# Kernel tuning notes

Measured on AMD Instinct MI355X. Metric: run time of the kernel, lower is better.

## Reference

```python
import jax, jax.numpy as jnp
import numpy as np

D_MODEL = 1024
NUM_HEADS = 16
DEPTH = D_MODEL // NUM_HEADS
B, S = 2, 2048


def setup_inputs() -> dict:
    key = jax.random.key(0)
    ks = jax.random.split(key, 13)
    sc = 1.0 / np.sqrt(D_MODEL)
    inp = {
        "q": jax.random.normal(ks[0], (B, S, D_MODEL), jnp.float32),
        "k": jax.random.normal(ks[1], (B, S, D_MODEL), jnp.float32),
        "v": jax.random.normal(ks[2], (B, S, D_MODEL), jnp.float32),
        "mask": jax.random.randint(ks[3], (B, 1, S, S), 0, 2).astype(jnp.float32),
        "wq": jax.random.normal(ks[4], (D_MODEL, D_MODEL), jnp.float32) * sc,
        "bq": jnp.zeros((D_MODEL,), jnp.float32),
        "wk": jax.random.normal(ks[5], (D_MODEL, D_MODEL), jnp.float32) * sc,
        "bk": jnp.zeros((D_MODEL,), jnp.float32),
        "wv": jax.random.normal(ks[6], (D_MODEL, D_MODEL), jnp.float32) * sc,
        "bv": jnp.zeros((D_MODEL,), jnp.float32),
        "wo": jax.random.normal(ks[7], (D_MODEL, D_MODEL), jnp.float32) * sc,
        "bo": jnp.zeros((D_MODEL,), jnp.float32),
    }
    return inp


def _split_heads(x):
    # [B,S,D] -> [B,H,S,depth]
    b, s, _ = x.shape
    return x.reshape(b, s, NUM_HEADS, DEPTH).transpose(0, 2, 1, 3)


def reference(q, k, v, mask, wq, bq, wk, bk, wv, bv, wo, bo):
    qh = _split_heads(q @ wq.T + bq)
    kh = _split_heads(k @ wk.T + bk)
    vh = _split_heads(v @ wv.T + bv)
    logits = jnp.einsum("bhqd,bhkd->bhqk", qh, kh) / jnp.sqrt(
        jnp.asarray(DEPTH, jnp.float32))
    logits = logits + mask * (-1e9)
    attn = jax.nn.softmax(logits, axis=-1)
    out = jnp.einsum("bhqk,bhkd->bhqd", attn, vh)
    out = out.transpose(0, 2, 1, 3).reshape(q.shape[0], -1, D_MODEL)
    return out @ wo.T + bo
```

## Files before the change

### kernel.cpp

```cpp
#include <hip/hip_runtime.h>

#define D_MODEL 1024
#define NHEADS  16
#define DEPTH   64
#define BATCH   2
#define SEQ     2048
#define MROWS   (BATCH * SEQ)
#define QSCALE  0.18033688011112042f

typedef unsigned short u16;
typedef unsigned int   u32;
typedef unsigned long long u64;
typedef __bf16 bf16x8 __attribute__((ext_vector_type(8)));
typedef float  f32x4  __attribute__((ext_vector_type(4)));

#if __has_builtin(__builtin_amdgcn_exp2f)
#define EXP2(x) __builtin_amdgcn_exp2f(x)
#else
#define EXP2(x) exp2f(x)
#endif

__device__ __forceinline__ u16 f2b(float f) {
    return __builtin_bit_cast(u16, static_cast<__bf16>(f));
}
__device__ __forceinline__ bf16x8 ldb8(const u16* p) {
    return __builtin_bit_cast(bf16x8, *(const uint4*)p);
}
__device__ __forceinline__ void gload16(const u16* g, u16* l) {
    __builtin_amdgcn_global_load_lds(
        (const __attribute__((address_space(1))) void*)g,
        (__attribute__((address_space(3))) void*)l, 16, 0, 0);
}

__global__ __launch_bounds__(256) void pack_mask(
    const float* __restrict__ mask, u64* __restrict__ bits)
{
    const int w    = blockIdx.x * 4 + (threadIdx.x >> 6);
    const int lane = threadIdx.x & 63;
    float m = mask[(size_t)w * 64 + lane];
    u64 b = __ballot(m > 0.5f);
    if (lane == 0) bits[w] = b;
}

__global__ __launch_bounds__(256) void cvt_pack(
    const float* __restrict__ q, const float* __restrict__ k, const float* __restrict__ v,
    const float* __restrict__ wq, const float* __restrict__ wk, const float* __restrict__ wv,
    const float* __restrict__ wo, const float* __restrict__ mask,
    u16* __restrict__ xb, u16* __restrict__ wb, u64* __restrict__ bits)
{
    if (blockIdx.x >= 8192) {
        const int w    = (blockIdx.x - 8192) * 4 + (threadIdx.x >> 6);
        const int lane = threadIdx.x & 63;
        float m = mask[(size_t)w * 64 + lane];
        u64 b = __ballot(m > 0.5f);
        if (lane == 0) bits[w] = b;
        return;
    }
    const size_t e = ((size_t)blockIdx.x * 256 + threadIdx.x) * 8;
    const float* src;
    u16* dst;
    size_t off;
    if (e < 12582912) {
        const int a = (int)(e >> 22);
        off = e & 4194303;
        src = (a == 0) ? q : (a == 1) ? k : v;
        dst = xb + ((size_t)a << 22) + off;
    } else {
        const size_t e2 = e - 12582912;
        const int a = (int)(e2 >> 20);
        off = e2 & 1048575;
        src = (a == 0) ? wq : (a == 1) ? wk : (a == 2) ? wv : wo;
        dst = wb + ((size_t)a << 20) + off;
    }
    const float4 f0 = *(const float4*)(src + off);
    const float4 f1 = *(const float4*)(src + off + 4);
    uint4 o;
    o.x = (u32)f2b(f0.x) | ((u32)f2b(f0.y) << 16);
    o.y = (u32)f2b(f0.z) | ((u32)f2b(f0.w) << 16);
    o.z = (u32)f2b(f1.x) | ((u32)f2b(f1.y) << 16);
    o.w = (u32)f2b(f1.z) | ((u32)f2b(f1.w) << 16);
    *(uint4*)dst = o;
}

__global__ __launch_bounds__(256, 3) void proj3_bf16(
    const u16* __restrict__ xb, const u16* __restrict__ wb,
    const float* __restrict__ bq, const float* __restrict__ bk, const float* __restrict__ bv,
    u16* __restrict__ qws, u16* __restrict__ kws, u16* __restrict__ vtws)
{
    __shared__ __align__(16) u16 smem[16384];
    u16 (*la)[4096] = reinterpret_cast<u16(*)[4096]>(smem);
    u16 (*lb)[4096] = reinterpret_cast<u16(*)[4096]>(smem + 8192);

    const int z = blockIdx.z;
    const u16* X = xb + ((size_t)z << 22);
    const u16* W = wb + ((size_t)z << 20);
    const float* Bi = (z == 0) ? bq : (z == 1) ? bk : bv;
    u16* dst       = (z == 0) ? qws : (z == 1) ? kws : vtws;

    const int tid  = threadIdx.x;
    const int wv_  = tid >> 6;
    const int lane = tid & 63;
    const int quad = lane >> 4;
    const int l15  = lane & 15;
    const int bx = blockIdx.y >> 2;
    const int by = (blockIdx.x << 2) | (blockIdx.y & 3);
    const int wm = (wv_ >> 1) * 64;
    const int wn = (wv_ & 1) * 64;

    f32x4 acc[4][4];
    for (int i = 0; i < 4; ++i)
        for (int j = 0; j < 4; ++j)
            acc[i][j] = (f32x4){0.f, 0.f, 0.f, 0.f};

    const int rowA0 = by * 128;
    const int rowB0 = bx * 128;

    const int strow = tid >> 2;
    const int stcol = (tid & 3) * 8;
    const u16* gA0 = &X[(size_t)(rowA0 + strow) * D_MODEL + stcol];
    const u16* gA1 = gA0 + (size_t)64 * D_MODEL;
    const u16* gB0 = &W[(size_t)(rowB0 + strow) * D_MODEL + stcol];
    const u16* gB1 = gB0 + (size_t)64 * D_MODEL;
    const int l0 = tid * 8, l1 = 2048 + tid * 8;

    gload16(gA0, &la[0][l0]);
    gload16(gA1, &la[0][l1]);
    gload16(gB0, &lb[0][l0]);
    gload16(gB1, &lb[0][l1]);
    __syncthreads();

    for (int t = 0; t < 32; ++t) {
        const int buf = t & 1;
        if (t < 31) {
            const int ko = (t + 1) * 32;
            gload16(gA0 + ko, &la[buf ^ 1][l0]);
            gload16(gA1 + ko, &la[buf ^ 1][l1]);
            gload16(gB0 + ko, &lb[buf ^ 1][l0]);
            gload16(gB1 + ko, &lb[buf ^ 1][l1]);
        }
        bf16x8 af[4], bfr[4];
        #pragma unroll
        for (int tt = 0; tt < 4; ++tt) {
            af[tt]  = ldb8(&la[buf][(wm + tt * 16 + l15) * 32 + quad * 8]);
            bfr[tt] = ldb8(&lb[buf][(wn + tt * 16 + l15) * 32 + quad * 8]);
        }
        #pragma unroll
        for (int mt = 0; mt < 4; ++mt)
            #pragma unroll
            for (int nt = 0; nt < 4; ++nt)
                acc[mt][nt] = __builtin_amdgcn_mfma_f32_16x16x32_bf16(af[mt], bfr[nt], acc[mt][nt], 0, 0, 0);
        __syncthreads();
    }

    if (z != 2) {
        #pragma unroll
        for (int nt = 0; nt < 4; ++nt) {
            int n = rowB0 + wn + nt * 16 + l15;
            float bvv = Bi[n];
            int h = n >> 6, d = n & 63;
            #pragma unroll
            for (int mt = 0; mt < 4; ++mt) {
                #pragma unroll
                for (int r = 0; r < 4; ++r) {
                    int m = rowA0 + wm + mt * 16 + quad * 4 + r;
                    float c = acc[mt][nt][r] + bvv;
                    if (z == 0) c *= QSCALE;
                    int b = m >> 11, s = m & (SEQ - 1);
                    dst[(((size_t)(b * NHEADS + h) * SEQ) + s) * DEPTH + d] = f2b(c);
                }
            }
        }
    } else {
        #pragma unroll
        for (int nt = 0; nt < 4; ++nt) {
            const int nl = wn + nt * 16 + l15;
            const float bvv = Bi[rowB0 + nl];
            #pragma unroll
            for (int mt = 0; mt < 4; ++mt) {
                #pragma unroll
                for (int r2 = 0; r2 < 4; r2 += 2) {
                    const int ml = wm + mt * 16 + quad * 4 + r2;
                    u32 pk = (u32)f2b(acc[mt][nt][r2] + bvv)
                           | ((u32)f2b(acc[mt][nt][r2 + 1] + bvv) << 16);
                    const int g = ml >> 3;
                    *(u32*)&smem[nl * 128 + (((g ^ (nl & 15)) << 3) | (ml & 7))] = pk;
                }
            }
        }
        __syncthreads();
        const int nl  = tid >> 1;
        const int cc0 = (tid & 1) * 64;
        const int n   = rowB0 + nl;
        const int bb  = rowA0 >> 11;
        u16* dbase = dst + (((size_t)(bb * NHEADS + (n >> 6)) * DEPTH) + (n & 63)) * SEQ
                   + (rowA0 & (SEQ - 1)) + cc0;
        #pragma unroll
        for (int j = 0; j < 8; ++j) {
            const int g = (tid & 1) * 8 + j;
            *(uint4*)&dbase[j * 8] =
                *(const uint4*)&smem[nl * 128 + ((g ^ (nl & 15)) << 3)];
        }
    }
}

__global__ __launch_bounds__(256, 3) void proj3_fused(
    const float* __restrict__ q, const float* __restrict__ k, const float* __restrict__ v,
    const float* __restrict__ wq, const float* __restrict__ wk, const float* __restrict__ wv,
    const float* __restrict__ bq, const float* __restrict__ bk, const float* __restrict__ bv,
    u16* __restrict__ qws, u16* __restrict__ kws, u16* __restrict__ vtws)
{
    __shared__ __align__(16) u16 ldsA[128 * 40];
    __shared__ __align__(16) u16 ldsB[128 * 40];

    const int z = blockIdx.z;
    const float* X  = (z == 0) ? q  : (z == 1) ? k  : v;
    const float* W  = (z == 0) ? wq : (z == 1) ? wk : wv;
    const float* Bi = (z == 0) ? bq : (z == 1) ? bk : bv;
    u16* dst        = (z == 0) ? qws : (z == 1) ? kws : vtws;

    const int tid  = threadIdx.x;
    const int wv_  = tid >> 6;
    const int lane = tid & 63;
    const int quad = lane >> 4;
    const int l15  = lane & 15;
    const int bx = blockIdx.y >> 2;
    const int by = (blockIdx.x << 2) | (blockIdx.y & 3);
    const int wm = (wv_ >> 1) * 64;
    const int wn = (wv_ & 1) * 64;

    f32x4 acc[4][4];
    for (int i = 0; i < 4; ++i)
        for (int j = 0; j < 4; ++j)
            acc[i][j] = (f32x4){0.f, 0.f, 0.f, 0.f};

    const int rowA0 = by * 128;
    const int rowB0 = bx * 128;

    const int sr = tid >> 3;
    const int sc = (tid & 7) * 4;

    float4 pa[4], pb[4];
    #pragma unroll
    for (int i = 0; i < 4; ++i) {
        pa[i] = *(const float4*)&X[(size_t)(rowA0 + sr + i * 32) * D_MODEL + sc];
        pb[i] = *(const float4*)&W[(size_t)(rowB0 + sr + i * 32) * D_MODEL + sc];
    }

    for (int it = 0; it < 32; ++it) {
        #pragma unroll
        for (int i = 0; i < 4; ++i) {
            ushort4 ha, hb;
            ha.x = f2b(pa[i].x); ha.y = f2b(pa[i].y); ha.z = f2b(pa[i].z); ha.w = f2b(pa[i].w);
            hb.x = f2b(pb[i].x); hb.y = f2b(pb[i].y); hb.z = f2b(pb[i].z); hb.w = f2b(pb[i].w);
            *(ushort4*)&ldsA[(sr + i * 32) * 40 + sc] = ha;
            *(ushort4*)&ldsB[(sr + i * 32) * 40 + sc] = hb;
        }
        __syncthreads();

        if (it < 31) {
            const int k0 = (it + 1) * 32;
            #pragma unroll
            for (int i = 0; i < 4; ++i) {
                pa[i] = *(const float4*)&X[(size_t)(rowA0 + sr + i * 32) * D_MODEL + k0 + sc];
                pb[i] = *(const float4*)&W[(size_t)(rowB0 + sr + i * 32) * D_MODEL + k0 + sc];
            }
        }

        bf16x8 af[4], bfr[4];
        #pragma unroll
        for (int t = 0; t < 4; ++t) {
            af[t]  = ldb8(&ldsA[(wm + t * 16 + l15) * 40 + quad * 8]);
            bfr[t] = ldb8(&ldsB[(wn + t * 16 + l15) * 40 + quad * 8]);
        }
        #pragma unroll
        for (int mt = 0; mt < 4; ++mt)
            #pragma unroll
            for (int nt = 0; nt < 4; ++nt)
                acc[mt][nt] = __builtin_amdgcn_mfma_f32_16x16x32_bf16(af[mt], bfr[nt], acc[mt][nt], 0, 0, 0);
        __syncthreads();
    }

    #pragma unroll
    for (int nt = 0; nt < 4; ++nt) {
        int n = bx * 128 + wn + nt * 16 + l15;
        float bvv = Bi[n];
        int h = n >> 6, d = n & 63;
        #pragma unroll
        for (int mt = 0; mt < 4; ++mt) {
            #pragma unroll
            for (int r = 0; r < 4; ++r) {
                int m = by * 128 + wm + mt * 16 + quad * 4 + r;
                float c = acc[mt][nt][r] + bvv;
                if (z == 0) c *= QSCALE;
                int b = m >> 11, s = m & (SEQ - 1);
                if (z != 2)
                    dst[(((size_t)(b * NHEADS + h) * SEQ) + s) * DEPTH + d] = f2b(c);
                else
                    dst[(((size_t)(b * NHEADS + h) * DEPTH) + d) * SEQ + s] = f2b(c);
            }
        }
    }
}

__global__ __launch_bounds__(256, 4) void gemm_out_bf16(
    const u16* __restrict__ X, const u16* __restrict__ W,
    const float* __restrict__ bias, float* __restrict__ out)
{
    __shared__ __align__(16) u16 la[2][64 * 32];
    __shared__ __align__(16) u16 lb[2][64 * 32];

    const int tid  = threadIdx.x;
    const int wv_  = tid >> 6;
    const int lane = tid & 63;
    const int quad = lane >> 4;
    const int l15  = lane & 15;
    const int mx = blockIdx.x;
    const int nx = blockIdx.y;
    const int wm = (wv_ >> 1) * 32;
    const int wn = (wv_ & 1) * 32;

    f32x4 acc[2][2];
    for (int i = 0; i < 2; ++i)
        for (int j = 0; j < 2; ++j)
            acc[i][j] = (f32x4){0.f, 0.f, 0.f, 0.f};

    const int rowA0 = mx * 64;
    const int rowB0 = nx * 64;

    const int strow = tid >> 2;
    const int stcol = (tid & 3) * 8;
    const u16* gA0 = &X[(size_t)(rowA0 + strow) * D_MODEL + stcol];
    const u16* gB0 = &W[(size_t)(rowB0 + strow) * D_MODEL + stcol];
    const int l0 = tid * 8;

    gload16(gA0, &la[0][l0]);
    gload16(gB0, &lb[0][l0]);
    __syncthreads();

    for (int t = 0; t < 32; ++t) {
        const int buf = t & 1;
        if (t < 31) {
            const int ko = (t + 1) * 32;
            gload16(gA0 + ko, &la[buf ^ 1][l0]);
            gload16(gB0 + ko, &lb[buf ^ 1][l0]);
        }
        bf16x8 af[2], bfr[2];
        #pragma unroll
        for (int tt = 0; tt < 2; ++tt) {
            af[tt]  = ldb8(&la[buf][(wm + tt * 16 + l15) * 32 + quad * 8]);
            bfr[tt] = ldb8(&lb[buf][(wn + tt * 16 + l15) * 32 + quad * 8]);
        }
        #pragma unroll
        for (int mt = 0; mt < 2; ++mt)
            #pragma unroll
            for (int nt = 0; nt < 2; ++nt)
                acc[mt][nt] = __builtin_amdgcn_mfma_f32_16x16x32_bf16(af[mt], bfr[nt], acc[mt][nt], 0, 0, 0);
        __syncthreads();
    }

    #pragma unroll
    for (int nt = 0; nt < 2; ++nt) {
        int n = rowB0 + wn + nt * 16 + l15;
        float bvv = bias[n];
        #pragma unroll
        for (int mt = 0; mt < 2; ++mt) {
            #pragma unroll
            for (int r = 0; r < 4; ++r) {
                int m = rowA0 + wm + mt * 16 + quad * 4 + r;
                out[(size_t)m * D_MODEL + n] = acc[mt][nt][r] + bvv;
            }
        }
    }
}

__global__ __launch_bounds__(256) void gemm_out_f32(
    const u16* __restrict__ X, const float* __restrict__ W,
    const float* __restrict__ bias, float* __restrict__ out)
{
    __shared__ __align__(16) u16 ldsA[128 * 40];
    __shared__ __align__(16) u16 ldsB[64 * 40];

    const int tid  = threadIdx.x;
    const int wv_  = tid >> 6;
    const int lane = tid & 63;
    const int quad = lane >> 4;
    const int l15  = lane & 15;
    const int bx = ((blockIdx.y >> 2) << 1) | (blockIdx.x >> 3);
    const int by = ((blockIdx.x & 7) << 2) | (blockIdx.y & 3);
    const int wm = (wv_ >> 1) * 64;
    const int wn = (wv_ & 1) * 32;

    f32x4 acc[4][2];
    for (int i = 0; i < 4; ++i)
        for (int j = 0; j < 2; ++j)
            acc[i][j] = (f32x4){0.f, 0.f, 0.f, 0.f};

    const int rowA0 = by * 128;
    const int rowB0 = bx * 64;

    const int ar = tid >> 2, akc = (tid & 3) * 8;
    const int br = tid >> 3, bc = (tid & 7) * 4;

    uint4  paA[2];
    float4 paB[2];
    #pragma unroll
    for (int i = 0; i < 2; ++i) {
        paA[i] = *(const uint4*)&X[(size_t)(rowA0 + ar + i * 64) * D_MODEL + akc];
        paB[i] = *(const float4*)&W[(size_t)(rowB0 + br + i * 32) * D_MODEL + bc];
    }

    for (int it = 0; it < 32; ++it) {
        #pragma unroll
        for (int i = 0; i < 2; ++i) {
            *(uint4*)&ldsA[(ar + i * 64) * 40 + akc] = paA[i];
            ushort4 hb;
            hb.x = f2b(paB[i].x); hb.y = f2b(paB[i].y); hb.z = f2b(paB[i].z); hb.w = f2b(paB[i].w);
            *(ushort4*)&ldsB[(br + i * 32) * 40 + bc] = hb;
        }
        __syncthreads();

        if (it < 31) {
            const int k0 = (it + 1) * 32;
            #pragma unroll
            for (int i = 0; i < 2; ++i) {
                paA[i] = *(const uint4*)&X[(size_t)(rowA0 + ar + i * 64) * D_MODEL + k0 + akc];
                paB[i] = *(const float4*)&W[(size_t)(rowB0 + br + i * 32) * D_MODEL + k0 + bc];
            }
        }

        bf16x8 af[4], bfr[2];
        #pragma unroll
        for (int t = 0; t < 4; ++t)
            af[t] = ldb8(&ldsA[(wm + t * 16 + l15) * 40 + quad * 8]);
        #pragma unroll
        for (int t = 0; t < 2; ++t)
            bfr[t] = ldb8(&ldsB[(wn + t * 16 + l15) * 40 + quad * 8]);
        #pragma unroll
        for (int mt = 0; mt < 4; ++mt)
            #pragma unroll
            for (int nt = 0; nt < 2; ++nt)
                acc[mt][nt] = __builtin_amdgcn_mfma_f32_16x16x32_bf16(af[mt], bfr[nt], acc[mt][nt], 0, 0, 0);
        __syncthreads();
    }

    #pragma unroll
    for (int nt = 0; nt < 2; ++nt) {
        int n = bx * 64 + wn + nt * 16 + l15;
        float bvv = bias[n];
        #pragma unroll
        for (int mt = 0; mt < 4; ++mt) {
            #pragma unroll
            for (int r = 0; r < 4; ++r) {
                int m = by * 128 + wm + mt * 16 + quad * 4 + r;
                out[(size_t)m * D_MODEL + n] = acc[mt][nt][r] + bvv;
            }
        }
    }
}

__global__ __launch_bounds__(256, 4) void flash_attn(
    const u16* __restrict__ Q, const u16* __restrict__ K,
    const u16* __restrict__ Vt, const u64* __restrict__ maskbits,
    u16* __restrict__ O)
{
    __shared__ __align__(16) u16 ldsK[2][64 * 64];
    __shared__ __align__(16) u16 ldsV[2][64 * 64];
    __shared__ __align__(16) u16 ldsP[4][16 * 64];

    const int tid  = threadIdx.x;
    const int wv_  = tid >> 6;
    const int lane = tid & 63;
    const int quad = lane >> 4;
    const int l15  = lane & 15;
    const int bh = ((blockIdx.x & 7) << 2) | (blockIdx.y & 3);
    const int qt = ((blockIdx.y >> 2) << 2) | (blockIdx.x >> 3);
    const int b  = bh >> 4, h = bh & 15;
    const int q0 = qt * 64 + wv_ * 16;

    const u16* Qb = Q  + (size_t)bh * SEQ * DEPTH;
    const u16* Kb = K  + (size_t)bh * SEQ * DEPTH;
    const u16* Vb = Vt + (size_t)bh * DEPTH * SEQ;
    const u64* MB = maskbits + (size_t)b * SEQ * (SEQ / 64);

    const int sr8  = tid >> 3;
    const int sg   = tid & 7;
    const int scol = ((sg ^ (sr8 & 7)) * 8);
    const u16* kS0 = &Kb[(size_t)sr8 * DEPTH + scol];
    const u16* kS1 = &Kb[(size_t)(sr8 + 32) * DEPTH + scol];
    const u16* vS0 = &Vb[(size_t)sr8 * SEQ + scol];
    const u16* vS1 = &Vb[(size_t)(sr8 + 32) * SEQ + scol];
    const int ld0 = tid * 8, ld1 = 2048 + tid * 8;

    const int xk0 = ((quad ^ (l15 & 7)) * 8);
    const int xk1 = (((4 + quad) ^ (l15 & 7)) * 8);

    bf16x8 aq0 = ldb8(&Qb[(q0 + l15) * DEPTH + quad * 8]);
    bf16x8 aq1 = ldb8(&Qb[(q0 + l15) * DEPTH + 32 + quad * 8]);

    bf16x8 vones;
    #pragma unroll
    for (int i = 0; i < 8; ++i) vones[i] = (__bf16)1.0f;

    f32x4 oa[4];
    for (int i = 0; i < 4; ++i) oa[i] = (f32x4){0.f, 0.f, 0.f, 0.f};
    f32x4 lacc = (f32x4){0.f, 0.f, 0.f, 0.f};

    u16* myP = ldsP[wv_];

    int wpq[4];
    #pragma unroll
    for (int cc = 0; cc < 4; ++cc) {
        const int g = cc * 2 + (quad >> 1);
        wpq[cc] = l15 * 64 + ((g ^ (l15 & 7)) * 8) + (quad & 1) * 4;
    }
    const int rp0 = l15 * 64 + ((quad ^ (l15 & 7)) * 8);
    const int rp1 = l15 * 64 + (((4 + quad) ^ (l15 & 7)) * 8);

    gload16(kS0, &ldsK[0][ld0]);
    gload16(kS1, &ldsK[0][ld1]);
    gload16(vS0, &ldsV[0][ld0]);
    gload16(vS1, &ldsV[0][ld1]);
    __syncthreads();

    for (int it = 0; it < 32; ++it) {
        const int buf = it & 1;
        const u16* Kl = ldsK[buf];
        const u16* Vl = ldsV[buf];

        if (it < 31) {
            const int kb2 = (it + 1) * 64;
            gload16(kS0 + (size_t)kb2 * DEPTH, &ldsK[buf ^ 1][ld0]);
            gload16(kS1 + (size_t)kb2 * DEPTH, &ldsK[buf ^ 1][ld1]);
            gload16(vS0 + kb2, &ldsV[buf ^ 1][ld0]);
            gload16(vS1 + kb2, &ldsV[buf ^ 1][ld1]);
        }

        const u64 t = MB[(size_t)(q0 + l15) * (SEQ / 64) + it];
        const u32 tlo = (u32)t, thi = (u32)(t >> 32);

        #pragma unroll
        for (int cc = 0; cc < 4; ++cc) {
            const int row = cc * 16 + l15;
            bf16x8 bk0 = ldb8(&Kl[row * 64 + xk0]);
            bf16x8 bk1 = ldb8(&Kl[row * 64 + xk1]);
            f32x4 z = (f32x4){0.f, 0.f, 0.f, 0.f};
            z = __builtin_amdgcn_mfma_f32_16x16x32_bf16(bk0, aq0, z, 0, 0, 0);
            z = __builtin_amdgcn_mfma_f32_16x16x32_bf16(bk1, aq1, z, 0, 0, 0);
            const u32 w = (cc & 2) ? thi : tlo;
            float p[4];
            #pragma unroll
            for (int r = 0; r < 4; ++r) {
                const u32 bit = (w >> ((cc & 1) * 16 + quad * 4 + r)) & 1u;
                float e = EXP2(z[r]);
                p[r] = bit ? 0.f : e;
            }
            uint2 pk;
            pk.x = (u32)f2b(p[0]) | ((u32)f2b(p[1]) << 16);
            pk.y = (u32)f2b(p[2]) | ((u32)f2b(p[3]) << 16);
            *(uint2*)&myP[wpq[cc]] = pk;
        }

        __builtin_amdgcn_wave_barrier();
        __builtin_amdgcn_s_waitcnt(0xc07f);
        __builtin_amdgcn_wave_barrier();
        bf16x8 pa0 = ldb8(&myP[rp0]);
        bf16x8 pa1 = ldb8(&myP[rp1]);

        lacc = __builtin_amdgcn_mfma_f32_16x16x32_bf16(pa0, vones, lacc, 0, 0, 0);
        lacc = __builtin_amdgcn_mfma_f32_16x16x32_bf16(pa1, vones, lacc, 0, 0, 0);

        #pragma unroll
        for (int n = 0; n < 4; ++n) {
            const int row = n * 16 + l15;
            bf16x8 bv0 = ldb8(&Vl[row * 64 + xk0]);
            bf16x8 bv1 = ldb8(&Vl[row * 64 + xk1]);
            oa[n] = __builtin_amdgcn_mfma_f32_16x16x32_bf16(pa0, bv0, oa[n], 0, 0, 0);
            oa[n] = __builtin_amdgcn_mfma_f32_16x16x32_bf16(pa1, bv1, oa[n], 0, 0, 0);
        }

        __syncthreads();
    }

    float inv[4];
    #pragma unroll
    for (int r = 0; r < 4; ++r)
        inv[r] = 1.0f / lacc[r];

    #pragma unroll
    for (int n = 0; n < 4; ++n)
        #pragma unroll
        for (int r = 0; r < 4; ++r) {
            int m = q0 + quad * 4 + r;
            O[((size_t)b * SEQ + m) * D_MODEL + h * DEPTH + n * 16 + l15] =
                f2b(oa[n][r] * inv[r]);
        }
}

extern "C" void kernel_launch(void* const* d_in, const int* in_sizes, int n_in,
                              void* d_out, int out_size, void* d_ws, size_t ws_size,
                              hipStream_t stream) {
    const float* q    = (const float*)d_in[0];
    const float* k    = (const float*)d_in[1];
    const float* v    = (const float*)d_in[2];
    const float* mask = (const float*)d_in[3];
    const float* wq   = (const float*)d_in[4];
    const float* bq   = (const float*)d_in[5];
    const float* wk   = (const float*)d_in[6];
    const float* bk   = (const float*)d_in[7];
    const float* wv   = (const float*)d_in[8];
    const float* bv   = (const float*)d_in[9];
    const float* wo   = (const float*)d_in[10];
    const float* bo   = (const float*)d_in[11];

    u16* base = (u16*)d_ws;
    const size_t seg = (size_t)BATCH * NHEADS * SEQ * DEPTH;
    u16* qws  = base;
    u16* kws  = base + seg;
    u16* vtws = base + 2 * seg;
    u16* ows  = base + 3 * seg;
    u64* mbits = (u64*)(base + 4 * seg);
    u16* wb   = base + 4 * seg + 524288;
    u16* xb   = wb + 4 * 1048576;
    const size_t need_bf16 = (4 * seg + 524288 + 4 * 1048576 + 3 * seg) * 2;
    const bool bf16path = (ws_size >= need_bf16);

    dim3 blk(256);
    dim3 gp(D_MODEL / 128, MROWS / 128, 3);
    if (bf16path) {
        hipLaunchKernelGGL(cvt_pack, dim3(8192 + 32768), blk, 0, stream,
                           q, k, v, wq, wk, wv, wo, mask, xb, wb, mbits);
        hipLaunchKernelGGL(proj3_bf16, gp, blk, 0, stream,
                           xb, wb, bq, bk, bv, qws, kws, vtws);
    } else {
        hipLaunchKernelGGL(pack_mask, dim3(BATCH * SEQ * (SEQ / 64) / 4), blk, 0, stream, mask, mbits);
        hipLaunchKernelGGL(proj3_fused, gp, blk, 0, stream,
                           q, k, v, wq, wk, wv, bq, bk, bv, qws, kws, vtws);
    }

    dim3 ga(32, 32);
    hipLaunchKernelGGL(flash_attn, ga, blk, 0, stream, qws, kws, vtws, mbits, ows);

    if (bf16path) {
        dim3 go(MROWS / 64, D_MODEL / 64);
        hipLaunchKernelGGL(gemm_out_bf16, go, blk, 0, stream, ows, wb + 3 * 1048576, bo, (float*)d_out);
    } else {
        dim3 go(D_MODEL / 64, MROWS / 128);
        hipLaunchKernelGGL(gemm_out_f32, go, blk, 0, stream, ows, wo, bo, (float*)d_out);
    }
}
```

Before: 270.5 us.

## Split attention tile into two halves interleaving QK/softmax with PV, add setprio

The 64-key tile per iteration is split into two 32-key halves. Each half computes QK^T and exp, writes P to LDS, then immediately runs its PV and row-sum MFMAs, so exp/VALU work from one half can overlap matrix work from the other. s_setprio raises wave priority around the MFMA groups. The P LDS addressing gets an extra XOR swizzle on lane parity to reduce bank conflicts. The cost is an extra intra-wave LDS wait per iteration and more complex scheduling.

```diff
diff --git a/kernel.cpp b/kernel.cpp
--- a/kernel.cpp
+++ b/kernel.cpp
@@ -507,14 +507,15 @@
 
     u16* myP = ldsP[wv_];
 
+    const int rpar = (l15 & 1) << 5;
     int wpq[4];
     #pragma unroll
     for (int cc = 0; cc < 4; ++cc) {
         const int g = cc * 2 + (quad >> 1);
-        wpq[cc] = l15 * 64 + ((g ^ (l15 & 7)) * 8) + (quad & 1) * 4;
-    }
-    const int rp0 = l15 * 64 + ((quad ^ (l15 & 7)) * 8);
-    const int rp1 = l15 * 64 + (((4 + quad) ^ (l15 & 7)) * 8);
+        wpq[cc] = l15 * 64 + ((((g ^ (l15 & 7)) * 8) + (quad & 1) * 4) ^ rpar);
+    }
+    const int rp0 = l15 * 64 + (((quad ^ (l15 & 7)) * 8) ^ rpar);
+    const int rp1 = l15 * 64 + ((((4 + quad) ^ (l15 & 7)) * 8) ^ rpar);
 
     gload16(kS0, &ldsK[0][ld0]);
     gload16(kS1, &ldsK[0][ld1]);
@@ -539,18 +540,19 @@
         const u32 tlo = (u32)t, thi = (u32)(t >> 32);
 
         #pragma unroll
-        for (int cc = 0; cc < 4; ++cc) {
+        for (int cc = 0; cc < 2; ++cc) {
             const int row = cc * 16 + l15;
             bf16x8 bk0 = ldb8(&Kl[row * 64 + xk0]);
             bf16x8 bk1 = ldb8(&Kl[row * 64 + xk1]);
             f32x4 z = (f32x4){0.f, 0.f, 0.f, 0.f};
+            __builtin_amdgcn_s_setprio(1);
             z = __builtin_amdgcn_mfma_f32_16x16x32_bf16(bk0, aq0, z, 0, 0, 0);
             z = __builtin_amdgcn_mfma_f32_16x16x32_bf16(bk1, aq1, z, 0, 0, 0);
-            const u32 w = (cc & 2) ? thi : tlo;
+            __builtin_amdgcn_s_setprio(0);
             float p[4];
             #pragma unroll
             for (int r = 0; r < 4; ++r) {
-                const u32 bit = (w >> ((cc & 1) * 16 + quad * 4 + r)) & 1u;
+                const u32 bit = (tlo >> ((cc & 1) * 16 + quad * 4 + r)) & 1u;
                 float e = EXP2(z[r]);
                 p[r] = bit ? 0.f : e;
             }
@@ -563,19 +565,56 @@
         __builtin_amdgcn_wave_barrier();
         __builtin_amdgcn_s_waitcnt(0xc07f);
         __builtin_amdgcn_wave_barrier();
-        bf16x8 pa0 = ldb8(&myP[rp0]);
-        bf16x8 pa1 = ldb8(&myP[rp1]);
-
-        lacc = __builtin_amdgcn_mfma_f32_16x16x32_bf16(pa0, vones, lacc, 0, 0, 0);
-        lacc = __builtin_amdgcn_mfma_f32_16x16x32_bf16(pa1, vones, lacc, 0, 0, 0);
-
-        #pragma unroll
-        for (int n = 0; n < 4; ++n) {
-            const int row = n * 16 + l15;
-            bf16x8 bv0 = ldb8(&Vl[row * 64 + xk0]);
-            bf16x8 bv1 = ldb8(&Vl[row * 64 + xk1]);
-            oa[n] = __builtin_amdgcn_mfma_f32_16x16x32_bf16(pa0, bv0, oa[n], 0, 0, 0);
-            oa[n] = __builtin_amdgcn_mfma_f32_16x16x32_bf16(pa1, bv1, oa[n], 0, 0, 0);
+        {
+            bf16x8 pa0 = ldb8(&myP[rp0]);
+            __builtin_amdgcn_s_setprio(1);
+            lacc = __builtin_amdgcn_mfma_f32_16x16x32_bf16(pa0, vones, lacc, 0, 0, 0);
+            #pragma unroll
+            for (int n = 0; n < 4; ++n) {
+                const int row = n * 16 + l15;
+                bf16x8 bv0 = ldb8(&Vl[row * 64 + xk0]);
+                oa[n] = __builtin_amdgcn_mfma_f32_16x16x32_bf16(pa0, bv0, oa[n], 0, 0, 0);
+            }
+            __builtin_amdgcn_s_setprio(0);
+        }
+
+        #pragma unroll
+        for (int cc = 2; cc < 4; ++cc) {
+            const int row = cc * 16 + l15;
+            bf16x8 bk0 = ldb8(&Kl[row * 64 + xk0]);
+            bf16x8 bk1 = ldb8(&Kl[row * 64 + xk1]);
+            f32x4 z = (f32x4){0.f, 0.f, 0.f, 0.f};
+            __builtin_amdgcn_s_setprio(1);
+            z = __builtin_amdgcn_mfma_f32_16x16x32_bf16(bk0, aq0, z, 0, 0, 0);
+            z = __builtin_amdgcn_mfma_f32_16x16x32_bf16(bk1, aq1, z, 0, 0, 0);
+            __builtin_amdgcn_s_setprio(0);
+            float p[4];
+            #pragma unroll
+            for (int r = 0; r < 4; ++r) {
+                const u32 bit = (thi >> ((cc & 1) * 16 + quad * 4 + r)) & 1u;
+                float e = EXP2(z[r]);
+                p[r] = bit ? 0.f : e;
+            }
+            uint2 pk;
+            pk.x = (u32)f2b(p[0]) | ((u32)f2b(p[1]) << 16);
+            pk.y = (u32)f2b(p[2]) | ((u32)f2b(p[3]) << 16);
+            *(uint2*)&myP[wpq[cc]] = pk;
+        }
+
+        __builtin_amdgcn_wave_barrier();
+        __builtin_amdgcn_s_waitcnt(0xc07f);
+        __builtin_amdgcn_wave_barrier();
+        {
+            bf16x8 pa1 = ldb8(&myP[rp1]);
+            __builtin_amdgcn_s_setprio(1);
+            lacc = __builtin_amdgcn_mfma_f32_16x16x32_bf16(pa1, vones, lacc, 0, 0, 0);
+            #pragma unroll
+            for (int n = 0; n < 4; ++n) {
+                const int row = n * 16 + l15;
+                bf16x8 bv1 = ldb8(&Vl[row * 64 + xk1]);
+                oa[n] = __builtin_amdgcn_mfma_f32_16x16x32_bf16(pa1, bv1, oa[n], 0, 0, 0);
+            }
+            __builtin_amdgcn_s_setprio(0);
         }
 
         __syncthreads();
```

Result: no change. 271.9 us (+0.5%).
